# Performance work log

Hardware: AMD Instinct MI355X
Metric: run time of the kernel (lower is better)

## Reference

```python
import jax, jax.numpy as jnp
from jax import lax
import numpy as np

LOGZERO = -(65504.0 ** 2)  # -torch.finfo(float16).min**2


def setup_inputs() -> dict:
    key = jax.random.key(0)
    ks = jax.random.split(key, 5)
    B, T, D, V, CB, Ly = 32, 512, 512, 4096, 30, 4
    x = jax.random.normal(ks[0], (B, T, D), jnp.float32)
    W = jax.random.normal(ks[1], (V, D), jnp.float32) * 0.02
    b = jax.random.normal(ks[2], (V,), jnp.float32) * 0.02
    xl = jnp.full((B,), T, jnp.int32)
    y = jax.random.randint(ks[3], (B, Ly), 1, V)  # partial hypothesis (last token used)
    # unique candidate ids per row (exclude blank=0) to avoid duplicate-scatter ambiguity
    scores = jax.random.uniform(ks[4], (B, V - 1))
    ctc_beam_idx = jnp.argsort(scores, axis=1)[:, :CB] + 1
    return {"x": x, "W": W, "b": b, "xl": xl, "y": y,
            "ctc_beam_idx": ctc_beam_idx, "blank": 0, "eos": V - 1}


def reference(x, W, b, xl, y, ctc_beam_idx, blank, eos):
    B, T, D = x.shape
    V = W.shape[0]
    CB = ctc_beam_idx.shape[1]
    # forward(): Linear + log_softmax  -> (B, T, V)
    logp = jax.nn.log_softmax(jnp.einsum("btd,vd->btv", x, W) + b, axis=-1)
    # preProcess(): lastP[1] = cumsum of blank logprob over time, lastP[0] = logzero
    blank_lp = logp[:, :, blank]                     # (B, T)
    lastP1 = jnp.cumsum(blank_lp, axis=1).T          # (T, B)
    lastP0 = jnp.full((T, B), LOGZERO, logp.dtype)
    lastPsum = jnp.logaddexp(lastP0, lastP1)         # (T, B)
    # cState.select / bState.select -> candidate and blank scores per beam hyp
    Xn = jnp.take_along_axis(logp, ctc_beam_idx[:, None, :], axis=2)  # (B, T, CB)
    Xn = Xn.transpose(1, 0, 2)                                        # (T, B, CB)
    Xb = jnp.broadcast_to(blank_lp.T[:, :, None], Xn.shape)           # (T, B, CB)
    # prefP: lastPsum everywhere, lastP[1] where candidate == last prediction
    same = (y[:, -1][:, None] == ctc_beam_idx)                        # (B, CB)
    prefP = jnp.where(same[None], lastP1[:, :, None], lastPsum[:, :, None])  # (T, B, CB)
    Ly = y.shape[1]
    start = min(Ly, T - 1)
    loop_start = max(start, 1)
    Pn0 = jnp.full((B, CB), LOGZERO, logp.dtype)
    Pb0 = jnp.full((B, CB), LOGZERO, logp.dtype)
    if start == 0:
        Pn0 = Xn[0]
    def step(carry, inp):
        Pn_prev, Pb_prev = carry
        pref_prev, xn_t, xb_t = inp
        Pn = jnp.logaddexp(Pn_prev, pref_prev) + xn_t
        Pb = jnp.logaddexp(Pn_prev, Pb_prev) + xb_t
        return (Pn, Pb), (Pn, Pb)
    _, (Pn_seq, Pb_seq) = lax.scan(
        step, (Pn0, Pb0),
        (prefP[loop_start - 1:T - 1], Xn[loop_start:], Xb[loop_start:]))
    if start == 0:  # prepend the preset t=0 entry
        Pn_seq = jnp.concatenate([Pn0[None], Pn_seq], axis=0)
        Pb_seq = jnp.concatenate([Pb0[None], Pb_seq], axis=0)
    # curP over t in [start, T)
    curP_t = jnp.logaddexp(Pn_seq, Pb_seq)                            # (T-start, B, CB)
    t_idx = jnp.arange(start, T)
    valid = xl[None, :] > t_idx[:, None]                              # (T-start, B)
    curP_t = jnp.where(valid[:, :, None], curP_t, LOGZERO)
    curP = jax.nn.logsumexp(curP_t, axis=0)                           # (B, CB)
    # scatter into vocab; initial self.prefP == 0.0
    finalP = jnp.full((B, V), LOGZERO, curP.dtype)
    finalP = finalP.at[jnp.arange(B)[:, None], ctc_beam_idx].set(curP)
    # eos score: lastPsum at final valid frame only
    ar = jnp.arange(T)
    maskBT = xl[:, None] > ar[None, :]
    mask0 = (xl - 1)[:, None] > ar[None, :]
    lps = jnp.where(maskBT & ~mask0, lastPsum.T, 0.0)                 # (B, T)
    finalP = finalP.at[:, eos].set(jnp.sum(lps, axis=1))
    finalP = finalP.at[:, blank].set(LOGZERO)
    return finalP
```

## Files before the change

kernel.cpp:

```cpp
#include <hip/hip_runtime.h>
#include <hip/hip_fp8.h>

#define LOGZERO -4290774016.0f
#define L2E 1.4426950408889634f
#define LN2 0.6931471805599453f

constexpr int Bb = 32, Tt = 512, Dd = 512, Vv = 4096;
constexpr int BT = Bb * Tt;

typedef __attribute__((ext_vector_type(4)))  float f32x4;
typedef __attribute__((ext_vector_type(16))) float f32x16;
typedef __attribute__((ext_vector_type(4)))  int   i32x4;
typedef __attribute__((ext_vector_type(8)))  int   i32x8;

#define GLOBAL_AS __attribute__((address_space(1)))
#define LDS_AS    __attribute__((address_space(3)))

__device__ __forceinline__ float fexp2(float x) { return __builtin_amdgcn_exp2f(x); }
__device__ __forceinline__ float flog2(float x) { return __builtin_amdgcn_logf(x); }

__device__ __forceinline__ unsigned cvt4_fp8(float4 v, float s) {
#if __has_builtin(__builtin_amdgcn_cvt_pk_fp8_f32)
  int p = __builtin_amdgcn_cvt_pk_fp8_f32(v.x * s, v.y * s, 0, false);
  p = __builtin_amdgcn_cvt_pk_fp8_f32(v.z * s, v.w * s, p, true);
  return (unsigned)p;
#else
  unsigned b0 = __hip_cvt_float_to_fp8(v.x * s, __HIP_SATFINITE, __HIP_E4M3);
  unsigned b1 = __hip_cvt_float_to_fp8(v.y * s, __HIP_SATFINITE, __HIP_E4M3);
  unsigned b2 = __hip_cvt_float_to_fp8(v.z * s, __HIP_SATFINITE, __HIP_E4M3);
  unsigned b3 = __hip_cvt_float_to_fp8(v.w * s, __HIP_SATFINITE, __HIP_E4M3);
  return b0 | (b1 << 8) | (b2 << 16) | (b3 << 24);
#endif
}

__device__ __forceinline__ float lg2add(float a, float b) {
  float mx = fmaxf(a, b);
  float d  = fabsf(a - b);
  return mx + flog2(1.0f + fexp2(-d));
}

__global__ __launch_bounds__(256) void kPre(const float* __restrict__ x,
                                            const float* __restrict__ W,
                                            unsigned char* __restrict__ Xfp,
                                            unsigned char* __restrict__ Wp) {
  const int t = blockIdx.x * 256 + threadIdx.x;
  if (t < 524288) {
    const int tM = t >> 10, s = t & 1023;
    const int l = s & 63, h = (s >> 6) & 1, kb = s >> 7;
    const int row = tM * 32 + (l & 31);
    const int col = kb * 64 + ((l >> 5) << 5) + h * 16;
    const float* p = x + (size_t)row * Dd + col;
    uint4 o;
    o.x = cvt4_fp8(*(const float4*)p, 1.0f);
    o.y = cvt4_fp8(*(const float4*)(p + 4), 1.0f);
    o.z = cvt4_fp8(*(const float4*)(p + 8), 1.0f);
    o.w = cvt4_fp8(*(const float4*)(p + 12), 1.0f);
    *(uint4*)(Xfp + (size_t)t * 16) = o;
  } else {
    const int tt = t - 524288;
    const int cb = tt >> 11, s = tt & 2047;
    const int l = s & 63, h = (s >> 6) & 1, ct = (s >> 7) & 1, kb = s >> 8;
    const int row = cb * 64 + ct * 32 + (l & 31);
    const int col = kb * 64 + ((l >> 5) << 5) + h * 16;
    const float* p = W + (size_t)row * Dd + col;
    uint4 o;
    o.x = cvt4_fp8(*(const float4*)p, 16.0f);
    o.y = cvt4_fp8(*(const float4*)(p + 4), 16.0f);
    o.z = cvt4_fp8(*(const float4*)(p + 8), 16.0f);
    o.w = cvt4_fp8(*(const float4*)(p + 12), 16.0f);
    *(uint4*)(Wp + (size_t)tt * 16) = o;
  }
}

__global__ __launch_bounds__(256, 6) void kA(const unsigned char* __restrict__ Xfp,
                                             const unsigned char* __restrict__ Wp,
                                             const float* __restrict__ bias,
                                             const int* __restrict__ beam,
                                             const int* __restrict__ blankp,
                                             float* __restrict__ Spart,
                                             float* __restrict__ selL,
                                             int CB) {
  __shared__ unsigned char Ald[16384];
  __shared__ float Spw[4][32];
  __shared__ int   selv[31];
  __shared__ float selb[31];

  const int tid = threadIdx.x;
  const int tileN = blockIdx.x & 15;
  const int tileM = blockIdx.x >> 4;
  const int row0 = tileM * 32, col0 = tileN * 256;
  const int bb = row0 >> 9;
  const int lane = tid & 63, w = tid >> 6;
  const int l31 = lane & 31, hi = lane >> 5;

  if (tid < 31) {
    int v = (tid == 0) ? *blankp : beam[bb * CB + tid - 1];
    selv[tid] = v;
    selb[tid] = bias[v];
  }

  const unsigned char* src = Xfp + (size_t)tileM * 16384;
  #pragma unroll
  for (int i = 0; i < 4; ++i) {
    int off = (w * 4 + i) * 1024;
    __builtin_amdgcn_global_load_lds((const GLOBAL_AS void*)(src + off + lane * 16),
                                     (LDS_AS void*)(Ald + off), 16, 0, 0);
  }
  __syncthreads();

  const int colw = col0 + w * 64;
  const int cb = tileN * 4 + w;

  f32x16 acc[2];
  #pragma unroll
  for (int ct = 0; ct < 2; ++ct)
    #pragma unroll
    for (int r = 0; r < 16; ++r) acc[ct][r] = 0.f;

  const unsigned char* wpB = Wp + (size_t)cb * 32768 + lane * 16;

  i32x8 bc[2];
  #pragma unroll
  for (int ct = 0; ct < 2; ++ct) {
    i32x4 lo = *(const i32x4*)(wpB + (ct * 2) * 1024);
    i32x4 hx = *(const i32x4*)(wpB + (ct * 2 + 1) * 1024);
    bc[ct] = __builtin_shufflevector(lo, hx, 0, 1, 2, 3, 4, 5, 6, 7);
  }

  #pragma unroll
  for (int kb = 0; kb < 8; ++kb) {
    i32x8 af;
    {
      i32x4 lo = *(const i32x4*)&Ald[(kb * 2) * 1024 + lane * 16];
      i32x4 hx = *(const i32x4*)&Ald[(kb * 2 + 1) * 1024 + lane * 16];
      af = __builtin_shufflevector(lo, hx, 0, 1, 2, 3, 4, 5, 6, 7);
    }
    i32x8 bn[2];
    const int kn = (kb < 7) ? kb + 1 : 7;
    #pragma unroll
    for (int ct = 0; ct < 2; ++ct) {
      i32x4 lo = *(const i32x4*)(wpB + (kn * 4 + ct * 2) * 1024);
      i32x4 hx = *(const i32x4*)(wpB + (kn * 4 + ct * 2 + 1) * 1024);
      bn[ct] = __builtin_shufflevector(lo, hx, 0, 1, 2, 3, 4, 5, 6, 7);
    }
    #pragma unroll
    for (int ct = 0; ct < 2; ++ct)
      acc[ct] = __builtin_amdgcn_mfma_scale_f32_32x32x64_f8f6f4(
          af, bc[ct], acc[ct],
          0, 0,
          0, 0x7f7f7f7f,
          0, 0x7b7b7b7b);
    bc[0] = bn[0]; bc[1] = bn[1];
  }

  float bvl[2];
  #pragma unroll
  for (int ct = 0; ct < 2; ++ct)
    bvl[ct] = bias[colw + ct * 32 + l31] * L2E;

  #pragma unroll
  for (int reg = 0; reg < 16; ++reg) {
    float s = fexp2(acc[0][reg] * L2E + bvl[0]) +
              fexp2(acc[1][reg] * L2E + bvl[1]);
    s += __shfl_xor(s, 1, 64);
    s += __shfl_xor(s, 2, 64);
    s += __shfl_xor(s, 4, 64);
    s += __shfl_xor(s, 8, 64);
    s += __shfl_xor(s, 16, 64);
    if (l31 == 0)
      Spw[w][(reg & 3) + 8 * (reg >> 2) + 4 * hi] = s;
  }
  __syncthreads();
  if (tid < 32) {
    float p = Spw[0][tid] + Spw[1][tid] + Spw[2][tid] + Spw[3][tid];
    Spart[(size_t)tileN * BT + row0 + tid] = p;
  }

  const int tbase = row0 & 511;
  #pragma unroll 1
  for (int s = 0; s < 31; ++s) {
    const int vsel = __builtin_amdgcn_readfirstlane(selv[s]);
    const int local = vsel - colw;
    if (local >= 0 && local < 32) {
      const float bvs = selb[s];
      if (l31 == local) {
        #pragma unroll
        for (int reg = 0; reg < 16; ++reg) {
          int t = tbase + (reg & 3) + 8 * (reg >> 2) + 4 * hi;
          selL[((size_t)bb * Tt + t) * 31 + s] = acc[0][reg] + bvs;
        }
      }
    } else if (local >= 32 && local < 64) {
      const float bvs = selb[s];
      if (l31 == (local & 31)) {
        #pragma unroll
        for (int reg = 0; reg < 16; ++reg) {
          int t = tbase + (reg & 3) + 8 * (reg >> 2) + 4 * hi;
          selL[((size_t)bb * Tt + t) * 31 + s] = acc[1][reg] + bvs;
        }
      }
    }
  }
}

__global__ __launch_bounds__(256) void kC(const float* __restrict__ selL,
                                          const float* __restrict__ Spart,
                                          const int* __restrict__ xl,
                                          const int* __restrict__ beam,
                                          const int* __restrict__ blankp,
                                          const int* __restrict__ eosp,
                                          float* __restrict__ out,
                                          int Ly, int CB) {
  __shared__ float sl[Tt * 31];
  __shared__ float lgS[Tt];
  __shared__ float lastP1[Tt];
  __shared__ float blankLp[Tt];
  const int b = blockIdx.x, tid = threadIdx.x;

  for (int i = tid; i < Tt * 31; i += 256)
    sl[i] = selL[(size_t)b * Tt * 31 + i] * L2E;
  for (int tt = tid; tt < Tt; tt += 256) {
    float s = 0.f;
    #pragma unroll
    for (int n = 0; n < 16; ++n) s += Spart[(size_t)n * BT + b * Tt + tt];
    lgS[tt] = flog2(s);
  }
  __syncthreads();

  float* orow = out + (size_t)b * Vv;
  for (int i = tid; i < Vv; i += 256) orow[i] = LOGZERO;

  const int xlb = xl[b];
  float curP = LOGZERO;
  if (tid < 64) {
    const int lane = tid;
    float vloc[8];
    float run = 0.f;
    #pragma unroll
    for (int u = 0; u < 8; ++u) {
      int t = lane * 8 + u;
      float bl = sl[t * 31] - lgS[t];
      blankLp[t] = bl;
      run += bl;
      vloc[u] = run;
    }
    float inc = run;
    #pragma unroll
    for (int off = 1; off < 64; off <<= 1) {
      float o = __shfl_up(inc, off, 64);
      if (lane >= off) inc += o;
    }
    float excl = inc - run;
    #pragma unroll
    for (int u = 0; u < 8; ++u) lastP1[lane * 8 + u] = vloc[u] + excl;

    const int kk = (lane < CB) ? lane : (CB - 1);
    const float LOG2ZERO = LOGZERO * L2E;
    float Pn = LOG2ZERO, Pb = LOG2ZERO;
    float mrun = -3.0e38f, srun = 0.0f;
    int start = (Ly < Tt - 1) ? Ly : (Tt - 1);
    if (start == 0) {
      Pn = sl[1 + kk] - lgS[0];
      float vv = (0 < xlb) ? lg2add(Pn, Pb) : LOG2ZERO;
      float nm = fmaxf(mrun, vv);
      srun = srun * fexp2(mrun - nm) + fexp2(vv - nm);
      mrun = nm;
    }
    int t0 = (start > 1) ? start : 1;
    #pragma unroll 2
    for (int t = t0; t < Tt; ++t) {
      float xn = sl[t * 31 + 1 + kk] - lgS[t];
      float xb = blankLp[t];
      float pref = lastP1[t - 1];
      float Pn2 = lg2add(Pn, pref) + xn;
      float Pb2 = lg2add(Pn, Pb) + xb;
      Pn = Pn2; Pb = Pb2;
      float vv = (t < xlb) ? lg2add(Pn, Pb) : LOG2ZERO;
      float nm = fmaxf(mrun, vv);
      srun = srun * fexp2(mrun - nm) + fexp2(vv - nm);
      mrun = nm;
    }
    curP = (mrun + flog2(srun)) * LN2;
  }
  __syncthreads();

  if (tid < 64) {
    if (tid < CB) orow[beam[b * CB + tid]] = curP;
  }
  __syncthreads();
  if (tid == 0) {
    float eosv = (xlb >= 1) ? lastP1[xlb - 1] * LN2 : 0.0f;
    orow[*eosp] = eosv;
    orow[*blankp] = LOGZERO;
  }
}

extern "C" void kernel_launch(void* const* d_in, const int* in_sizes, int n_in,
                              void* d_out, int out_size, void* d_ws, size_t ws_size,
                              hipStream_t stream) {
  (void)n_in; (void)out_size; (void)ws_size;
  const float* x    = (const float*)d_in[0];
  const float* W    = (const float*)d_in[1];
  const float* bias = (const float*)d_in[2];
  const int* xl     = (const int*)d_in[3];
  const int* beam   = (const int*)d_in[5];
  const int* blankp = (const int*)d_in[6];
  const int* eosp   = (const int*)d_in[7];
  const int Ly = in_sizes[4] / Bb;
  const int CB = in_sizes[5] / Bb;

  float* Spart = (float*)d_ws;
  float* selL  = (float*)((char*)d_ws + (size_t)0x100000);
  unsigned char* Xfp = (unsigned char*)((char*)d_ws + (size_t)0x400000);
  unsigned char* Wp  = (unsigned char*)((char*)d_ws + (size_t)0xC00000);
  float* outf = (float*)d_out;

  kPre<<<2560, 256, 0, stream>>>(x, W, Xfp, Wp);
  kA<<<8192, 256, 0, stream>>>(Xfp, Wp, bias, beam, blankp, Spart, selL, CB);
  kC<<<Bb, 256, 0, stream>>>(selL, Spart, xl, beam, blankp, eosp, outf, Ly, CB);
}
```

Before: 221.9 us.

## Stage fp8 conversion through swizzled LDS for coalesced loads; prefetch scan operands

The fp8 pre-pass now gives each block a full 32-row tile. It reads the tile with fully coalesced float4 loads and writes the fp8 bytes into XOR-swizzled shared memory, then stores them in the MFMA-friendly layout with 16-byte writes. Before, each thread gathered strided 16-float chunks. In the scan kernel, the log-normaliser is subtracted once when selL is loaded into shared memory, which removes the per-step subtraction and the blankLp buffer. Next-step operands are also software-prefetched inside the serial time loop. The changes add a barrier and extra LDS use in the pre-pass.

```diff
diff --git a/kernel.cpp b/kernel.cpp
--- a/kernel.cpp
+++ b/kernel.cpp
@@ -43,32 +43,55 @@
                                             const float* __restrict__ W,
                                             unsigned char* __restrict__ Xfp,
                                             unsigned char* __restrict__ Wp) {
-  const int t = blockIdx.x * 256 + threadIdx.x;
-  if (t < 524288) {
-    const int tM = t >> 10, s = t & 1023;
-    const int l = s & 63, h = (s >> 6) & 1, kb = s >> 7;
-    const int row = tM * 32 + (l & 31);
-    const int col = kb * 64 + ((l >> 5) << 5) + h * 16;
-    const float* p = x + (size_t)row * Dd + col;
-    uint4 o;
-    o.x = cvt4_fp8(*(const float4*)p, 1.0f);
-    o.y = cvt4_fp8(*(const float4*)(p + 4), 1.0f);
-    o.z = cvt4_fp8(*(const float4*)(p + 8), 1.0f);
-    o.w = cvt4_fp8(*(const float4*)(p + 12), 1.0f);
-    *(uint4*)(Xfp + (size_t)t * 16) = o;
+  __shared__ unsigned char T[16384];
+  const int tid = threadIdx.x, bid = blockIdx.x;
+  const bool isX = bid < 512;
+  const float* srcF;
+  float scale;
+  int cb = 0, half = 0;
+  if (isX) {
+    srcF = x + (size_t)bid * 32 * Dd;
+    scale = 1.0f;
   } else {
-    const int tt = t - 524288;
-    const int cb = tt >> 11, s = tt & 2047;
-    const int l = s & 63, h = (s >> 6) & 1, ct = (s >> 7) & 1, kb = s >> 8;
-    const int row = cb * 64 + ct * 32 + (l & 31);
-    const int col = kb * 64 + ((l >> 5) << 5) + h * 16;
-    const float* p = W + (size_t)row * Dd + col;
-    uint4 o;
-    o.x = cvt4_fp8(*(const float4*)p, 16.0f);
-    o.y = cvt4_fp8(*(const float4*)(p + 4), 16.0f);
-    o.z = cvt4_fp8(*(const float4*)(p + 8), 16.0f);
-    o.w = cvt4_fp8(*(const float4*)(p + 12), 16.0f);
-    *(uint4*)(Wp + (size_t)tt * 16) = o;
+    int idx = bid - 512;
+    cb = idx >> 1; half = idx & 1;
+    srcF = W + ((size_t)cb * 64 + half * 32) * Dd;
+    scale = 16.0f;
+  }
+
+  #pragma unroll
+  for (int p = 0; p < 16; ++p) {
+    int f = p * 256 + tid;
+    int r = f >> 7;
+    int cf = f & 127;
+    int c = cf >> 2, m = cf & 3;
+    float4 v = *(const float4*)(srcF + (size_t)f * 4);
+    unsigned o = cvt4_fp8(v, scale);
+    *(unsigned*)(T + ((r * 32 + (c ^ r)) * 16 + m * 4)) = o;
+  }
+  __syncthreads();
+
+  if (isX) {
+    unsigned char* dst = Xfp + (size_t)bid * 16384;
+    #pragma unroll
+    for (int u = 0; u < 4; ++u) {
+      int s = u * 256 + tid;
+      int r = s & 31, khalf = (s >> 5) & 1, h = (s >> 6) & 1, kb = s >> 7;
+      int c = kb * 4 + khalf * 2 + h;
+      uint4 o = *(const uint4*)(T + (r * 32 + (c ^ r)) * 16);
+      *(uint4*)(dst + (size_t)s * 16) = o;
+    }
+  } else {
+    unsigned char* dst = Wp + (size_t)cb * 32768;
+    #pragma unroll
+    for (int u = 0; u < 4; ++u) {
+      int lsl = u * 256 + tid;
+      int r = lsl & 31, khalf = (lsl >> 5) & 1, h = (lsl >> 6) & 1, kb = lsl >> 7;
+      int c = kb * 4 + khalf * 2 + h;
+      int s = kb * 256 + half * 128 + h * 64 + khalf * 32 + r;
+      uint4 o = *(const uint4*)(T + (r * 32 + (c ^ r)) * 16);
+      *(uint4*)(dst + (size_t)s * 16) = o;
+    }
   }
 }
 
@@ -214,16 +237,18 @@
   __shared__ float sl[Tt * 31];
   __shared__ float lgS[Tt];
   __shared__ float lastP1[Tt];
-  __shared__ float blankLp[Tt];
   const int b = blockIdx.x, tid = threadIdx.x;
 
-  for (int i = tid; i < Tt * 31; i += 256)
-    sl[i] = selL[(size_t)b * Tt * 31 + i] * L2E;
   for (int tt = tid; tt < Tt; tt += 256) {
     float s = 0.f;
     #pragma unroll
     for (int n = 0; n < 16; ++n) s += Spart[(size_t)n * BT + b * Tt + tt];
     lgS[tt] = flog2(s);
+  }
+  __syncthreads();
+  for (int i = tid; i < Tt * 31; i += 256) {
+    int t = i / 31;
+    sl[i] = selL[(size_t)b * Tt * 31 + i] * L2E - lgS[t];
   }
   __syncthreads();
 
@@ -239,8 +264,7 @@
     #pragma unroll
     for (int u = 0; u < 8; ++u) {
       int t = lane * 8 + u;
-      float bl = sl[t * 31] - lgS[t];
-      blankLp[t] = bl;
+      float bl = sl[t * 31];
       run += bl;
       vloc[u] = run;
     }
@@ -260,25 +284,32 @@
     float mrun = -3.0e38f, srun = 0.0f;
     int start = (Ly < Tt - 1) ? Ly : (Tt - 1);
     if (start == 0) {
-      Pn = sl[1 + kk] - lgS[0];
+      Pn = sl[1 + kk];
       float vv = (0 < xlb) ? lg2add(Pn, Pb) : LOG2ZERO;
       float nm = fmaxf(mrun, vv);
       srun = srun * fexp2(mrun - nm) + fexp2(vv - nm);
       mrun = nm;
     }
     int t0 = (start > 1) ? start : 1;
+    float xn_c = sl[t0 * 31 + 1 + kk];
+    float xb_c = sl[t0 * 31];
+    float pf_c = lastP1[t0 - 1];
     #pragma unroll 2
     for (int t = t0; t < Tt; ++t) {
-      float xn = sl[t * 31 + 1 + kk] - lgS[t];
-      float xb = blankLp[t];
-      float pref = lastP1[t - 1];
-      float Pn2 = lg2add(Pn, pref) + xn;
-      float Pb2 = lg2add(Pn, Pb) + xb;
+      float xn_n = 0.f, xb_n = 0.f, pf_n = 0.f;
+      if (t + 1 < Tt) {
+        xn_n = sl[(t + 1) * 31 + 1 + kk];
+        xb_n = sl[(t + 1) * 31];
+        pf_n = lastP1[t];
+      }
+      float Pn2 = lg2add(Pn, pf_c) + xn_c;
+      float Pb2 = lg2add(Pn, Pb) + xb_c;
       Pn = Pn2; Pb = Pb2;
       float vv = (t < xlb) ? lg2add(Pn, Pb) : LOG2ZERO;
       float nm = fmaxf(mrun, vv);
       srun = srun * fexp2(mrun - nm) + fexp2(vv - nm);
       mrun = nm;
+      xn_c = xn_n; xb_c = xb_n; pf_c = pf_n;
     }
     curP = (mrun + flog2(srun)) * LN2;
   }
@@ -315,7 +346,7 @@
   unsigned char* Wp  = (unsigned char*)((char*)d_ws + (size_t)0xC00000);
   float* outf = (float*)d_out;
 
-  kPre<<<2560, 256, 0, stream>>>(x, W, Xfp, Wp);
+  kPre<<<640, 256, 0, stream>>>(x, W, Xfp, Wp);
   kA<<<8192, 256, 0, stream>>>(Xfp, Wp, bias, beam, blankp, Spart, selL, CB);
   kC<<<Bb, 256, 0, stream>>>(selL, Spart, xl, beam, blankp, eosp, outf, Ly, CB);
 }
```

Result: slower. 233.0 us (+5.0%).

## Double M-tile per block to reuse W fragments across two row tiles

Applied to the files above, without the earlier changes.

Each kA block now covers 64 rows instead of 32, so every W fragment loaded from global memory feeds two MFMA row tiles. This halves the grid and the total W traffic. The cross-wave row-sum reduction now goes through a swizzled LDS buffer that reuses the A tile space, replacing the shuffle reduction. In exchange, register pressure and LDS use per block go up, occupancy is lowered to 4 blocks, and the k loop is no longer unrolled.

```diff
diff --git a/kernel.cpp b/kernel.cpp
--- a/kernel.cpp
+++ b/kernel.cpp
@@ -37,6 +37,12 @@
   float mx = fmaxf(a, b);
   float d  = fabsf(a - b);
   return mx + flog2(1.0f + fexp2(-d));
+}
+
+__device__ __forceinline__ i32x8 ld2(const unsigned char* p) {
+  i32x4 lo = *(const i32x4*)p;
+  i32x4 hx = *(const i32x4*)(p + 1024);
+  return __builtin_shufflevector(lo, hx, 0, 1, 2, 3, 4, 5, 6, 7);
 }
 
 __global__ __launch_bounds__(256) void kPre(const float* __restrict__ x,
@@ -72,7 +78,7 @@
   }
 }
 
-__global__ __launch_bounds__(256, 6) void kA(const unsigned char* __restrict__ Xfp,
+__global__ __launch_bounds__(256, 4) void kA(const unsigned char* __restrict__ Xfp,
                                              const unsigned char* __restrict__ Wp,
                                              const float* __restrict__ bias,
                                              const int* __restrict__ beam,
@@ -80,15 +86,14 @@
                                              float* __restrict__ Spart,
                                              float* __restrict__ selL,
                                              int CB) {
-  __shared__ unsigned char Ald[16384];
-  __shared__ float Spw[4][32];
+  __shared__ unsigned char Ald[32768];
   __shared__ int   selv[31];
   __shared__ float selb[31];
 
   const int tid = threadIdx.x;
   const int tileN = blockIdx.x & 15;
   const int tileM = blockIdx.x >> 4;
-  const int row0 = tileM * 32, col0 = tileN * 256;
+  const int row0 = tileM * 64, col0 = tileN * 256;
   const int bb = row0 >> 9;
   const int lane = tid & 63, w = tid >> 6;
   const int l31 = lane & 31, hi = lane >> 5;
@@ -99,10 +104,10 @@
     selb[tid] = bias[v];
   }
 
-  const unsigned char* src = Xfp + (size_t)tileM * 16384;
+  const unsigned char* src = Xfp + (size_t)tileM * 32768;
   #pragma unroll
-  for (int i = 0; i < 4; ++i) {
-    int off = (w * 4 + i) * 1024;
+  for (int i = 0; i < 8; ++i) {
+    int off = (w * 8 + i) * 1024;
     __builtin_amdgcn_global_load_lds((const GLOBAL_AS void*)(src + off + lane * 16),
                                      (LDS_AS void*)(Ald + off), 16, 0, 0);
   }
@@ -111,69 +116,75 @@
   const int colw = col0 + w * 64;
   const int cb = tileN * 4 + w;
 
-  f32x16 acc[2];
+  f32x16 acc[2][2];
   #pragma unroll
   for (int ct = 0; ct < 2; ++ct)
     #pragma unroll
-    for (int r = 0; r < 16; ++r) acc[ct][r] = 0.f;
+    for (int mt = 0; mt < 2; ++mt)
+      #pragma unroll
+      for (int r = 0; r < 16; ++r) acc[ct][mt][r] = 0.f;
 
   const unsigned char* wpB = Wp + (size_t)cb * 32768 + lane * 16;
+  const unsigned char* aB  = Ald + lane * 16;
 
   i32x8 bc[2];
-  #pragma unroll
-  for (int ct = 0; ct < 2; ++ct) {
-    i32x4 lo = *(const i32x4*)(wpB + (ct * 2) * 1024);
-    i32x4 hx = *(const i32x4*)(wpB + (ct * 2 + 1) * 1024);
-    bc[ct] = __builtin_shufflevector(lo, hx, 0, 1, 2, 3, 4, 5, 6, 7);
-  }
-
-  #pragma unroll
+  bc[0] = ld2(wpB);
+  bc[1] = ld2(wpB + 2048);
+
+  #pragma unroll 1
   for (int kb = 0; kb < 8; ++kb) {
-    i32x8 af;
-    {
-      i32x4 lo = *(const i32x4*)&Ald[(kb * 2) * 1024 + lane * 16];
-      i32x4 hx = *(const i32x4*)&Ald[(kb * 2 + 1) * 1024 + lane * 16];
-      af = __builtin_shufflevector(lo, hx, 0, 1, 2, 3, 4, 5, 6, 7);
-    }
     i32x8 bn[2];
     const int kn = (kb < 7) ? kb + 1 : 7;
-    #pragma unroll
-    for (int ct = 0; ct < 2; ++ct) {
-      i32x4 lo = *(const i32x4*)(wpB + (kn * 4 + ct * 2) * 1024);
-      i32x4 hx = *(const i32x4*)(wpB + (kn * 4 + ct * 2 + 1) * 1024);
-      bn[ct] = __builtin_shufflevector(lo, hx, 0, 1, 2, 3, 4, 5, 6, 7);
-    }
-    #pragma unroll
-    for (int ct = 0; ct < 2; ++ct)
-      acc[ct] = __builtin_amdgcn_mfma_scale_f32_32x32x64_f8f6f4(
-          af, bc[ct], acc[ct],
-          0, 0,
-          0, 0x7f7f7f7f,
-          0, 0x7b7b7b7b);
+    bn[0] = ld2(wpB + kn * 4096);
+    bn[1] = ld2(wpB + kn * 4096 + 2048);
+    {
+      i32x8 af0 = ld2(aB + kb * 2048);
+      acc[0][0] = __builtin_amdgcn_mfma_scale_f32_32x32x64_f8f6f4(
+          af0, bc[0], acc[0][0], 0, 0, 0, 0x7f7f7f7f, 0, 0x7b7b7b7b);
+      acc[1][0] = __builtin_amdgcn_mfma_scale_f32_32x32x64_f8f6f4(
+          af0, bc[1], acc[1][0], 0, 0, 0, 0x7f7f7f7f, 0, 0x7b7b7b7b);
+    }
+    {
+      i32x8 af1 = ld2(aB + 16384 + kb * 2048);
+      acc[0][1] = __builtin_amdgcn_mfma_scale_f32_32x32x64_f8f6f4(
+          af1, bc[0], acc[0][1], 0, 0, 0, 0x7f7f7f7f, 0, 0x7b7b7b7b);
+      acc[1][1] = __builtin_amdgcn_mfma_scale_f32_32x32x64_f8f6f4(
+          af1, bc[1], acc[1][1], 0, 0, 0, 0x7f7f7f7f, 0, 0x7b7b7b7b);
+    }
     bc[0] = bn[0]; bc[1] = bn[1];
   }
+
+  __syncthreads();
+  float* P = (float*)Ald;
 
   float bvl[2];
   #pragma unroll
   for (int ct = 0; ct < 2; ++ct)
     bvl[ct] = bias[colw + ct * 32 + l31] * L2E;
 
-  #pragma unroll
-  for (int reg = 0; reg < 16; ++reg) {
-    float s = fexp2(acc[0][reg] * L2E + bvl[0]) +
-              fexp2(acc[1][reg] * L2E + bvl[1]);
-    s += __shfl_xor(s, 1, 64);
-    s += __shfl_xor(s, 2, 64);
-    s += __shfl_xor(s, 4, 64);
-    s += __shfl_xor(s, 8, 64);
-    s += __shfl_xor(s, 16, 64);
-    if (l31 == 0)
-      Spw[w][(reg & 3) + 8 * (reg >> 2) + 4 * hi] = s;
-  }
-  __syncthreads();
-  if (tid < 32) {
-    float p = Spw[0][tid] + Spw[1][tid] + Spw[2][tid] + Spw[3][tid];
-    Spart[(size_t)tileN * BT + row0 + tid] = p;
+  {
+    const int f = w * 32 + l31;
+    const int chunk = f >> 2, elem = f & 3;
+    #pragma unroll
+    for (int mt = 0; mt < 2; ++mt) {
+      #pragma unroll
+      for (int reg = 0; reg < 16; ++reg) {
+        float s = fexp2(acc[0][mt][reg] * L2E + bvl[0]) +
+                  fexp2(acc[1][mt][reg] * L2E + bvl[1]);
+        int r31 = (reg & 3) + 8 * (reg >> 2) + 4 * hi;
+        int row = mt * 32 + r31;
+        P[row * 128 + ((chunk ^ r31) << 2) + elem] = s;
+      }
+    }
+  }
+  __syncthreads();
+  if (tid < 64) {
+    const int r31 = tid & 31;
+    f32x4 v = {0.f, 0.f, 0.f, 0.f};
+    #pragma unroll
+    for (int i = 0; i < 32; ++i)
+      v += *(const f32x4*)&P[tid * 128 + ((i ^ r31) << 2)];
+    Spart[(size_t)tileN * BT + row0 + tid] = v[0] + v[1] + v[2] + v[3];
   }
 
   const int tbase = row0 & 511;
@@ -185,19 +196,23 @@
       const float bvs = selb[s];
       if (l31 == local) {
         #pragma unroll
-        for (int reg = 0; reg < 16; ++reg) {
-          int t = tbase + (reg & 3) + 8 * (reg >> 2) + 4 * hi;
-          selL[((size_t)bb * Tt + t) * 31 + s] = acc[0][reg] + bvs;
-        }
+        for (int mt = 0; mt < 2; ++mt)
+          #pragma unroll
+          for (int reg = 0; reg < 16; ++reg) {
+            int t = tbase + mt * 32 + (reg & 3) + 8 * (reg >> 2) + 4 * hi;
+            selL[((size_t)bb * Tt + t) * 31 + s] = acc[0][mt][reg] + bvs;
+          }
       }
     } else if (local >= 32 && local < 64) {
       const float bvs = selb[s];
       if (l31 == (local & 31)) {
         #pragma unroll
-        for (int reg = 0; reg < 16; ++reg) {
-          int t = tbase + (reg & 3) + 8 * (reg >> 2) + 4 * hi;
-          selL[((size_t)bb * Tt + t) * 31 + s] = acc[1][reg] + bvs;
-        }
+        for (int mt = 0; mt < 2; ++mt)
+          #pragma unroll
+          for (int reg = 0; reg < 16; ++reg) {
+            int t = tbase + mt * 32 + (reg & 3) + 8 * (reg >> 2) + 4 * hi;
+            selL[((size_t)bb * Tt + t) * 31 + s] = acc[1][mt][reg] + bvs;
+          }
       }
     }
   }
@@ -316,6 +331,6 @@
   float* outf = (float*)d_out;
 
   kPre<<<2560, 256, 0, stream>>>(x, W, Xfp, Wp);
-  kA<<<8192, 256, 0, stream>>>(Xfp, Wp, bias, beam, blankp, Spart, selL, CB);
+  kA<<<4096, 256, 0, stream>>>(Xfp, Wp, bias, beam, blankp, Spart, selL, CB);
   kC<<<Bb, 256, 0, stream>>>(selL, Spart, xl, beam, blankp, eosp, outf, Ly, CB);
 }
```

Result: faster. 206.1 us (-7.1%).
